# Kernel optimization log

Hardware: AMD Instinct MI355X
Metric: run time of the kernel (lower is better)

The kernel has to match this reference:

```python
import jax, jax.numpy as jnp
import numpy as np
import math

B, T, C, H = 4, 1024, 1024, 16
D = C // H
EPS = 1e-5

def layer_norm(x, gamma, beta):
    mu = jnp.mean(x, axis=-1, keepdims=True)
    var = jnp.var(x, axis=-1, keepdims=True)
    return (x - mu) * jax.lax.rsqrt(var + EPS) * gamma + beta

def setup_inputs() -> dict:
    key = jax.random.key(0)
    ks = jax.random.split(key, 12)
    s = 0.02
    return {
        "x": jax.random.normal(ks[0], (B, T, C), dtype=jnp.float32),
        "attn_mask": jax.random.randint(ks[1], (B, 1, 1, T), 0, 2, dtype=jnp.int32),
        "Wq": jax.random.normal(ks[2], (C, C), dtype=jnp.float32) * s,
        "bq": jnp.zeros((C,), dtype=jnp.float32),
        "Wk": jax.random.normal(ks[3], (C, C), dtype=jnp.float32) * s,
        "bk": jnp.zeros((C,), dtype=jnp.float32),
        "Wv": jax.random.normal(ks[4], (C, C), dtype=jnp.float32) * s,
        "bv": jnp.zeros((C,), dtype=jnp.float32),
        "Wo": jax.random.normal(ks[5], (C, C), dtype=jnp.float32) * s,
        "bo": jnp.zeros((C,), dtype=jnp.float32),
        "ln_g": jnp.ones((C,), dtype=jnp.float32),
        "ln_b": jnp.zeros((C,), dtype=jnp.float32),
    }

def reference(x, attn_mask, Wq, bq, Wk, bk, Wv, bv, Wo, bo, ln_g, ln_b):
    # projections -> [B, H, T, D]
    def split_heads(y):
        return y.reshape(B, T, H, D).transpose(0, 2, 1, 3)
    q = split_heads(x @ Wq + bq)
    k = split_heads(x @ Wk + bk)
    v = split_heads(x @ Wv + bv)
    scale = 1.0 / math.sqrt(D)
    wei = jnp.einsum('bhqd,bhkd->bhqk', q, k) * scale  # [B,H,T,T]
    wei = jnp.where(attn_mask == 0, jnp.float32(-jnp.inf), wei)
    wei = jax.nn.softmax(wei, axis=-1)
    out = jnp.einsum('bhqk,bhkd->bhqd', wei, v)
    out = out.transpose(0, 2, 1, 3).reshape(B, T, C)
    out = out @ Wo + bo
    return layer_norm(out, ln_g, ln_b)
```

## Files before the change

kernel.cpp:

```cpp
#include <hip/hip_runtime.h>
#include <hip/hip_bf16.h>
#include <stdint.h>

#define B_ 4
#define T_ 1024
#define C_ 1024
#define H_ 16
#define D_ 64
#define M_ 4096

typedef __attribute__((ext_vector_type(8))) short bf16x8;
typedef __attribute__((ext_vector_type(4))) float f32x4;
typedef __attribute__((ext_vector_type(4))) short short4v;

static __device__ __forceinline__ short f2bf(float f) {
  union { float f; unsigned u; } c; c.f = f;
  unsigned r = (c.u + 0x7fffu + ((c.u >> 16) & 1u)) >> 16;
  return (short)(unsigned short)r;
}

static __device__ __forceinline__ void gl2lds16(const void* g, void* l) {
  __builtin_amdgcn_global_load_lds(
      (const __attribute__((address_space(1))) void*)(uintptr_t)g,
      (__attribute__((address_space(3))) void*)(uint32_t)(uintptr_t)l,
      16, 0, 0);
}

__global__ __launch_bounds__(256) void k_prep(
    const float* __restrict__ x, short* __restrict__ xb,
    const float* __restrict__ Wq, const float* __restrict__ Wk,
    const float* __restrict__ Wv, const float* __restrict__ Wo,
    short* __restrict__ Wt) {
  __shared__ float t[32][33];
  const int id = blockIdx.x, tid = threadIdx.x;
  if (id < 4096) {
    int i = id * 256 + tid;
    float4 v = ((const float4*)x)[i];
    short4v o;
    o.x = f2bf(v.x); o.y = f2bf(v.y); o.z = f2bf(v.z); o.w = f2bf(v.w);
    ((short4v*)xb)[i] = o;
    return;
  }
  int j = id - 4096;
  int bz = j >> 10, r = j & 1023;
  int by = r >> 5, bx = r & 31;
  const float* W = (bz == 0) ? Wq : (bz == 1) ? Wk : (bz == 2) ? Wv : Wo;
  short* out = Wt + (size_t)bz * C_ * C_;
  int n0 = bx * 32, k0 = by * 32;
  int tx = tid & 31, ty = tid >> 5;
#pragma unroll
  for (int i = 0; i < 4; i++)
    t[ty + 8*i][tx] = W[(size_t)(k0 + ty + 8*i) * C_ + n0 + tx];
  __syncthreads();
#pragma unroll
  for (int i = 0; i < 4; i++)
    out[(size_t)(n0 + ty + 8*i) * C_ + k0 + tx] = f2bf(t[tx][ty + 8*i]);
}

static __device__ __forceinline__ void gemm_body(const short* __restrict__ A,
                                                 const short* __restrict__ Bt,
                                                 short* sA, short* sB,
                                                 f32x4 acc[4][4], int m0, int n0) {
  const int tid = threadIdx.x;
  const int w = tid >> 6, lane = tid & 63;
  const int quad = lane >> 4, l16 = lane & 15;
  const int wm = (w >> 1) * 64, wn = (w & 1) * 64;
  const int srow = lane >> 3;
  const int sch = lane & 7;

#pragma unroll
  for (int mt = 0; mt < 4; mt++)
#pragma unroll
    for (int nt = 0; nt < 4; nt++)
#pragma unroll
      for (int e = 0; e < 4; e++) acc[mt][nt][e] = 0.f;

  for (int k0 = 0; k0 < C_; k0 += 64) {
    __syncthreads();
#pragma unroll
    for (int i = 0; i < 4; i++) {
      int c = w * 4 + i;
      int row = c * 8 + srow;
      int ch = sch ^ (row & 7);
      gl2lds16(&A[(size_t)(m0 + row) * C_ + k0 + ch * 8], &sA[c * 512]);
      gl2lds16(&Bt[(size_t)(n0 + row) * C_ + k0 + ch * 8], &sB[c * 512]);
    }
    __syncthreads();
#pragma unroll
    for (int ks = 0; ks < 2; ks++) {
      bf16x8 af[4], bfv[4];
      int chq = ks * 4 + quad;
#pragma unroll
      for (int t4 = 0; t4 < 4; t4++) {
        int rowa = wm + t4 * 16 + l16;
        af[t4] = *(const bf16x8*)&sA[rowa * 64 + (chq ^ (rowa & 7)) * 8];
        int rowb = wn + t4 * 16 + l16;
        bfv[t4] = *(const bf16x8*)&sB[rowb * 64 + (chq ^ (rowb & 7)) * 8];
      }
#pragma unroll
      for (int mt = 0; mt < 4; mt++)
#pragma unroll
        for (int nt = 0; nt < 4; nt++)
          acc[mt][nt] = __builtin_amdgcn_mfma_f32_16x16x32_bf16(
              af[mt], bfv[nt], acc[mt][nt], 0, 0, 0);
    }
  }
}

__global__ __launch_bounds__(256, 3) void k_qkv(
    const short* __restrict__ A, const short* __restrict__ WtAll,
    const float* __restrict__ bq, const float* __restrict__ bk,
    const float* __restrict__ bv,
    short* __restrict__ Qb, short* __restrict__ Kb, short* __restrict__ Vtb) {
  __shared__ short sU[17408];
  const int id = blockIdx.x;
  const int mode = id % 3;
  const int j = id / 3;
  const int bx = j & 7, by = j >> 3;
  const int m0 = by * 128, n0 = bx * 128;
  const short* Bt = WtAll + (size_t)mode * C_ * C_;
  const float* bias = (mode == 0) ? bq : (mode == 1) ? bk : bv;
  f32x4 acc[4][4];
  gemm_body(A, Bt, sU, sU + 8192, acc, m0, n0);

  const int tid = threadIdx.x;
  const int w = tid >> 6, lane = tid & 63;
  const int quad = lane >> 4, l16 = lane & 15;
  const int wm = (w >> 1) * 64, wn = (w & 1) * 64;

  __syncthreads();
  if (mode < 2) {
#pragma unroll
    for (int nt = 0; nt < 4; nt++) {
      int nl = wn + nt * 16 + l16;
      float bval = bias[n0 + nl];
#pragma unroll
      for (int mt = 0; mt < 4; mt++)
#pragma unroll
        for (int r = 0; r < 4; r++)
          sU[(wm + mt * 16 + quad * 4 + r) * 136 + nl] = f2bf(acc[mt][nt][r] + bval);
    }
    __syncthreads();
    int dr = tid >> 1, hf = tid & 1;
    int mg = m0 + dr;
    int bb = mg >> 10, t = mg & 1023;
    int h = (n0 >> 6) + hf;
    short* dst = (mode == 0) ? Qb : Kb;
    size_t base = ((((size_t)(bb * H_ + h)) << 10) + t) * D_;
#pragma unroll
    for (int i = 0; i < 8; i++)
      *(int4*)&dst[base + i * 8] = *(const int4*)&sU[dr * 136 + hf * 64 + i * 8];
  } else {
#pragma unroll
    for (int nt = 0; nt < 4; nt++) {
      int nl = wn + nt * 16 + l16;
      float bval = bias[n0 + nl];
#pragma unroll
      for (int mt = 0; mt < 4; mt++)
#pragma unroll
        for (int r = 0; r < 4; r++)
          sU[nl * 136 + wm + mt * 16 + quad * 4 + r] = f2bf(acc[mt][nt][r] + bval);
    }
    __syncthreads();
    int dr = tid >> 1;
    int dg = n0 + dr, hd = dg >> 6, dl = dg & 63;
    int bb2 = m0 >> 10, t0 = m0 & 1023;
    size_t base = (((size_t)(bb2 * H_ + hd) * D_ + dl) << 10) + t0;
#pragma unroll
    for (int i = 0; i < 8; i++) {
      int jj = (tid & 1) * 8 + i;
      *(int4*)&Vtb[base + jj * 8] = *(const int4*)&sU[dr * 136 + jj * 8];
    }
  }
}

__global__ __launch_bounds__(256, 3) void k_proj(
    const short* __restrict__ A, const short* __restrict__ Bt,
    const float* __restrict__ bias, float* __restrict__ Y) {
  __shared__ short sA[4096];
  __shared__ short sB[8192];
  const int tid = threadIdx.x;
  const int w = tid >> 6, lane = tid & 63;
  const int quad = lane >> 4, l16 = lane & 15;
  const int m0 = blockIdx.y * 64, n0 = blockIdx.x * 128;
  const int wm = (w >> 1) * 32, wn = (w & 1) * 64;
  const int srow = lane >> 3, sch = lane & 7;

  f32x4 acc[2][4];
#pragma unroll
  for (int mt = 0; mt < 2; mt++)
#pragma unroll
    for (int nt = 0; nt < 4; nt++)
#pragma unroll
      for (int e = 0; e < 4; e++) acc[mt][nt][e] = 0.f;

  for (int k0 = 0; k0 < C_; k0 += 64) {
    __syncthreads();
#pragma unroll
    for (int i = 0; i < 6; i++) {
      int c = w * 6 + i;
      if (c < 8) {
        int row = c * 8 + srow;
        int ch = sch ^ (row & 7);
        gl2lds16(&A[(size_t)(m0 + row) * C_ + k0 + ch * 8], &sA[c * 512]);
      } else {
        int c2 = c - 8;
        int row = c2 * 8 + srow;
        int ch = sch ^ (row & 7);
        gl2lds16(&Bt[(size_t)(n0 + row) * C_ + k0 + ch * 8], &sB[c2 * 512]);
      }
    }
    __syncthreads();
#pragma unroll
    for (int ks = 0; ks < 2; ks++) {
      bf16x8 af[2], bfv[4];
      int chq = ks * 4 + quad;
#pragma unroll
      for (int t2 = 0; t2 < 2; t2++) {
        int rowa = wm + t2 * 16 + l16;
        af[t2] = *(const bf16x8*)&sA[rowa * 64 + (chq ^ (rowa & 7)) * 8];
      }
#pragma unroll
      for (int t4 = 0; t4 < 4; t4++) {
        int rowb = wn + t4 * 16 + l16;
        bfv[t4] = *(const bf16x8*)&sB[rowb * 64 + (chq ^ (rowb & 7)) * 8];
      }
#pragma unroll
      for (int mt = 0; mt < 2; mt++)
#pragma unroll
        for (int nt = 0; nt < 4; nt++)
          acc[mt][nt] = __builtin_amdgcn_mfma_f32_16x16x32_bf16(
              af[mt], bfv[nt], acc[mt][nt], 0, 0, 0);
    }
  }

#pragma unroll
  for (int mt = 0; mt < 2; mt++)
#pragma unroll
    for (int nt = 0; nt < 4; nt++) {
      int ng = n0 + wn + nt * 16 + l16;
      float bval = bias[ng];
#pragma unroll
      for (int r = 0; r < 4; r++) {
        int mg = m0 + wm + mt * 16 + quad * 4 + r;
        Y[(size_t)mg * C_ + ng] = acc[mt][nt][r] + bval;
      }
    }
}

#define PSTRIDE 136
__global__ __launch_bounds__(256, 2) void k_attn(
    const short* __restrict__ Qb, const short* __restrict__ Kb,
    const short* __restrict__ Vtb, const int* __restrict__ mask,
    short* __restrict__ Ob) {
  __shared__ short sK[8192];
  __shared__ short sV[8192];
  __shared__ short sP[4 * 32 * PSTRIDE];
  __shared__ float sBias[1024];
  const int tid = threadIdx.x;
  const int w = tid >> 6, lane = tid & 63;
  const int quad = lane >> 4, l16 = lane & 15;

  const int bx = blockIdx.x;
  const int xcd = bx & 7, j = bx >> 3;
  const int qb = j & 7, u = j >> 3;
  const int h = xcd * 2 + (u & 1), bb = u >> 1;
  const int tq0 = qb * 128 + w * 32;

  const short* Qh = Qb + ((size_t)(bb * H_ + h) << 10) * D_;
  const short* Kh = Kb + ((size_t)(bb * H_ + h) << 10) * D_;
  const short* Vh = Vtb + (((size_t)(bb * H_ + h) * D_) << 10);
  const int* mrow = mask + bb * T_;
  short* Pw = &sP[w * 32 * PSTRIDE];

  const float SC = 0.125f * 1.44269504088896340736f;

  {
    int4 m4 = ((const int4*)mrow)[tid];
    float4 bv4;
    bv4.x = m4.x ? 0.f : -1e30f; bv4.y = m4.y ? 0.f : -1e30f;
    bv4.z = m4.z ? 0.f : -1e30f; bv4.w = m4.w ? 0.f : -1e30f;
    ((float4*)sBias)[tid] = bv4;
  }

  bf16x8 aq[2][2];
#pragma unroll
  for (int rt = 0; rt < 2; rt++)
#pragma unroll
    for (int ks = 0; ks < 2; ks++)
      aq[rt][ks] = *(const bf16x8*)&Qh[(size_t)(tq0 + rt * 16 + l16) * D_ +
                                       ks * 32 + quad * 8];

  bf16x8 ones8;
#pragma unroll
  for (int e = 0; e < 8; e++) ones8[e] = (short)0x3F80;

  f32x4 o[2][4];
  f32x4 osum[2];
#pragma unroll
  for (int rt = 0; rt < 2; rt++) {
#pragma unroll
    for (int nt = 0; nt < 4; nt++)
#pragma unroll
      for (int e = 0; e < 4; e++) o[rt][nt][e] = 0.f;
#pragma unroll
    for (int e = 0; e < 4; e++) osum[rt][e] = 0.f;
  }

  for (int kt = 0; kt < T_; kt += 128) {
    __syncthreads();
#pragma unroll
    for (int i2 = 0; i2 < 4; i2++) {
      int i = w * 4 + i2;
      int row = i * 8 + (lane >> 3);
      int g = (lane & 7) ^ (row & 7);
      gl2lds16(&Kh[(size_t)(kt + row) * D_ + g * 8], &sK[i * 512]);
    }
#pragma unroll
    for (int i2 = 0; i2 < 4; i2++) {
      int i = w * 4 + i2;
      int row = i * 4 + (lane >> 4);
      int g = (lane & 15) ^ (row & 15);
      gl2lds16(&Vh[((size_t)row << 10) + kt + g * 8], &sV[i * 512]);
    }
    __syncthreads();

    f32x4 s[2][8];
#pragma unroll
    for (int rt = 0; rt < 2; rt++)
#pragma unroll
      for (int ct = 0; ct < 8; ct++)
#pragma unroll
        for (int e = 0; e < 4; e++) s[rt][ct][e] = 0.f;

#pragma unroll
    for (int ks = 0; ks < 2; ks++)
#pragma unroll
      for (int ct = 0; ct < 8; ct++) {
        int rowb = ct * 16 + l16;
        bf16x8 bk8 = *(const bf16x8*)&sK[rowb * 64 +
                                         (((ks * 4 + quad) ^ (rowb & 7)) * 8)];
        s[0][ct] = __builtin_amdgcn_mfma_f32_16x16x32_bf16(aq[0][ks], bk8, s[0][ct], 0, 0, 0);
        s[1][ct] = __builtin_amdgcn_mfma_f32_16x16x32_bf16(aq[1][ks], bk8, s[1][ct], 0, 0, 0);
      }

    float mb[8];
#pragma unroll
    for (int ct = 0; ct < 8; ct++) mb[ct] = sBias[kt + ct * 16 + l16];

#pragma unroll
    for (int rt = 0; rt < 2; rt++)
#pragma unroll
      for (int ct = 0; ct < 8; ct++) {
        float p0 = __builtin_amdgcn_exp2f(fmaf(s[rt][ct][0], SC, mb[ct]));
        float p1 = __builtin_amdgcn_exp2f(fmaf(s[rt][ct][1], SC, mb[ct]));
        float p2 = __builtin_amdgcn_exp2f(fmaf(s[rt][ct][2], SC, mb[ct]));
        float p3 = __builtin_amdgcn_exp2f(fmaf(s[rt][ct][3], SC, mb[ct]));
        __hip_bfloat162 h01 = __float22bfloat162_rn(make_float2(p0, p1));
        __hip_bfloat162 h23 = __float22bfloat162_rn(make_float2(p2, p3));
        unsigned u01 = *(unsigned*)&h01;
        unsigned u23 = *(unsigned*)&h23;
        int base = (rt * 16 + quad * 4) * PSTRIDE + ct * 16 + l16;
        Pw[base] = (short)(u01 & 0xffffu);
        Pw[base + PSTRIDE] = (short)(u01 >> 16);
        Pw[base + 2 * PSTRIDE] = (short)(u23 & 0xffffu);
        Pw[base + 3 * PSTRIDE] = (short)(u23 >> 16);
      }

#pragma unroll
    for (int ks2 = 0; ks2 < 4; ks2++) {
      bf16x8 pa0 = *(const bf16x8*)&Pw[l16 * PSTRIDE + ks2 * 32 + quad * 8];
      bf16x8 pa1 = *(const bf16x8*)&Pw[(16 + l16) * PSTRIDE + ks2 * 32 + quad * 8];
      osum[0] = __builtin_amdgcn_mfma_f32_16x16x32_bf16(pa0, ones8, osum[0], 0, 0, 0);
      osum[1] = __builtin_amdgcn_mfma_f32_16x16x32_bf16(pa1, ones8, osum[1], 0, 0, 0);
#pragma unroll
      for (int nt = 0; nt < 4; nt++) {
        int rowv = nt * 16 + l16;
        bf16x8 bv8 = *(const bf16x8*)&sV[rowv * 128 +
                                         (((ks2 * 4 + quad) ^ (rowv & 15)) * 8)];
        o[0][nt] = __builtin_amdgcn_mfma_f32_16x16x32_bf16(pa0, bv8, o[0][nt], 0, 0, 0);
        o[1][nt] = __builtin_amdgcn_mfma_f32_16x16x32_bf16(pa1, bv8, o[1][nt], 0, 0, 0);
      }
    }
  }

#pragma unroll
  for (int rt = 0; rt < 2; rt++)
#pragma unroll
    for (int r = 0; r < 4; r++) {
      float inv = 1.f / osum[rt][r];
      int tg = tq0 + rt * 16 + quad * 4 + r;
#pragma unroll
      for (int nt = 0; nt < 4; nt++) {
        int col = h * D_ + nt * 16 + l16;
        Ob[(size_t)(bb * T_ + tg) * C_ + col] = f2bf(o[rt][nt][r] * inv);
      }
    }
}

__global__ __launch_bounds__(256) void k_ln(float* __restrict__ Y,
                                            const float* __restrict__ g,
                                            const float* __restrict__ b) {
  const int w = threadIdx.x >> 6, lane = threadIdx.x & 63;
  const int row = blockIdx.x * 4 + w;
  float4* yp = (float4*)(Y + (size_t)row * C_);
  float4 v[4];
#pragma unroll
  for (int i = 0; i < 4; i++) v[i] = yp[i * 64 + lane];

  float sm = 0.f;
#pragma unroll
  for (int i = 0; i < 4; i++) sm += v[i].x + v[i].y + v[i].z + v[i].w;
#pragma unroll
  for (int off = 32; off; off >>= 1) sm += __shfl_xor(sm, off);
  float mu = sm * (1.f / C_);

  float q = 0.f;
#pragma unroll
  for (int i = 0; i < 4; i++) {
    float dx = v[i].x - mu, dy = v[i].y - mu, dz = v[i].z - mu, dw = v[i].w - mu;
    q += dx * dx + dy * dy + dz * dz + dw * dw;
  }
#pragma unroll
  for (int off = 32; off; off >>= 1) q += __shfl_xor(q, off);
  float rsq = rsqrtf(q * (1.f / C_) + 1e-5f);

#pragma unroll
  for (int i = 0; i < 4; i++) {
    float4 gg = ((const float4*)g)[i * 64 + lane];
    float4 bb = ((const float4*)b)[i * 64 + lane];
    float4 out;
    out.x = (v[i].x - mu) * rsq * gg.x + bb.x;
    out.y = (v[i].y - mu) * rsq * gg.y + bb.y;
    out.z = (v[i].z - mu) * rsq * gg.z + bb.z;
    out.w = (v[i].w - mu) * rsq * gg.w + bb.w;
    yp[i * 64 + lane] = out;
  }
}

extern "C" void kernel_launch(void* const* d_in, const int* in_sizes, int n_in,
                              void* d_out, int out_size, void* d_ws, size_t ws_size,
                              hipStream_t stream) {
  (void)in_sizes; (void)n_in; (void)out_size; (void)ws_size;
  const float* x    = (const float*)d_in[0];
  const int*   mask = (const int*)d_in[1];
  const float* Wq   = (const float*)d_in[2];
  const float* bq   = (const float*)d_in[3];
  const float* Wk   = (const float*)d_in[4];
  const float* bk   = (const float*)d_in[5];
  const float* Wv   = (const float*)d_in[6];
  const float* bv   = (const float*)d_in[7];
  const float* Wo   = (const float*)d_in[8];
  const float* bo   = (const float*)d_in[9];
  const float* lng  = (const float*)d_in[10];
  const float* lnb  = (const float*)d_in[11];

  char* ws = (char*)d_ws;
  short* xb  = (short*)(ws);
  short* Wt  = (short*)(ws + ((size_t)8  << 20));
  short* Qb  = (short*)(ws + ((size_t)16 << 20));
  short* Kb  = (short*)(ws + ((size_t)24 << 20));
  short* Vtb = (short*)(ws + ((size_t)32 << 20));
  short* Ob  = xb;
  float* Y   = (float*)d_out;

  k_prep<<<dim3(8192), dim3(256), 0, stream>>>(x, xb, Wq, Wk, Wv, Wo, Wt);
  k_qkv<<<dim3(768), dim3(256), 0, stream>>>(xb, Wt, bq, bk, bv, Qb, Kb, Vtb);
  k_attn<<<dim3(512), dim3(256), 0, stream>>>(Qb, Kb, Vtb, mask, Ob);
  k_proj<<<dim3(8, 64), dim3(256), 0, stream>>>(Ob, Wt + (size_t)3 * C_ * C_, bo, Y);
  k_ln<<<dim3(1024), dim3(256), 0, stream>>>(Y, lng, lnb);
}
```

Measured before the change: 183.3 us.

## Compact unmasked keys and values to skip masked attention tiles

Computes a prefix-sum compaction of the key mask in the prep kernel, then gathers only unmasked K and V rows into compacted buffers. The attention loop then runs only over the padded count of valid keys, roughly halving the work for a random mask. This adds an extra gather kernel and an indirect-indexed V gather that reads scattered elements.

```diff
diff --git a/kernel.cpp b/kernel.cpp
--- a/kernel.cpp
+++ b/kernel.cpp
@@ -30,8 +30,10 @@
     const float* __restrict__ x, short* __restrict__ xb,
     const float* __restrict__ Wq, const float* __restrict__ Wk,
     const float* __restrict__ Wv, const float* __restrict__ Wo,
-    short* __restrict__ Wt) {
+    short* __restrict__ Wt, const int* __restrict__ mask,
+    int* __restrict__ tmap, float* __restrict__ bc, int* __restrict__ np) {
   __shared__ float t[32][33];
+  __shared__ int wsum[4];
   const int id = blockIdx.x, tid = threadIdx.x;
   if (id < 4096) {
     int i = id * 256 + tid;
@@ -41,20 +43,94 @@
     ((short4v*)xb)[i] = o;
     return;
   }
-  int j = id - 4096;
-  int bz = j >> 10, r = j & 1023;
-  int by = r >> 5, bx = r & 31;
-  const float* W = (bz == 0) ? Wq : (bz == 1) ? Wk : (bz == 2) ? Wv : Wo;
-  short* out = Wt + (size_t)bz * C_ * C_;
-  int n0 = bx * 32, k0 = by * 32;
-  int tx = tid & 31, ty = tid >> 5;
-#pragma unroll
-  for (int i = 0; i < 4; i++)
-    t[ty + 8*i][tx] = W[(size_t)(k0 + ty + 8*i) * C_ + n0 + tx];
+  if (id < 8192) {
+    int j = id - 4096;
+    int bz = j >> 10, r = j & 1023;
+    int by = r >> 5, bx = r & 31;
+    const float* W = (bz == 0) ? Wq : (bz == 1) ? Wk : (bz == 2) ? Wv : Wo;
+    short* out = Wt + (size_t)bz * C_ * C_;
+    int n0 = bx * 32, k0 = by * 32;
+    int tx = tid & 31, ty = tid >> 5;
+#pragma unroll
+    for (int i = 0; i < 4; i++)
+      t[ty + 8*i][tx] = W[(size_t)(k0 + ty + 8*i) * C_ + n0 + tx];
+    __syncthreads();
+#pragma unroll
+    for (int i = 0; i < 4; i++)
+      out[(size_t)(n0 + ty + 8*i) * C_ + k0 + tx] = f2bf(t[tx][ty + 8*i]);
+    return;
+  }
+  const int b = id - 8192;
+  const int lane = tid & 63, w = tid >> 6;
+  int4 m = ((const int4*)(mask + b * T_))[tid];
+  int cnt = (m.x ? 1 : 0) + (m.y ? 1 : 0) + (m.z ? 1 : 0) + (m.w ? 1 : 0);
+  int v = cnt;
+#pragma unroll
+  for (int off = 1; off < 64; off <<= 1) {
+    int u = __shfl_up(v, off);
+    if (lane >= off) v += u;
+  }
+  if (lane == 63) wsum[w] = v;
+  int4 z4; z4.x = 0; z4.y = 0; z4.z = 0; z4.w = 0;
+  ((int4*)(tmap + b * T_))[tid] = z4;
+  float4 neg; neg.x = -1e30f; neg.y = -1e30f; neg.z = -1e30f; neg.w = -1e30f;
+  ((float4*)(bc + b * T_))[tid] = neg;
   __syncthreads();
-#pragma unroll
-  for (int i = 0; i < 4; i++)
-    out[(size_t)(n0 + ty + 8*i) * C_ + k0 + tx] = f2bf(t[tx][ty + 8*i]);
+  int base = 0;
+#pragma unroll
+  for (int i = 0; i < 4; i++) if (i < w) base += wsum[i];
+  int incl = base + v;
+  int c = incl - cnt;
+  int t0 = tid * 4;
+  if (m.x) { tmap[b * T_ + c] = t0;     bc[b * T_ + c] = 0.f; c++; }
+  if (m.y) { tmap[b * T_ + c] = t0 + 1; bc[b * T_ + c] = 0.f; c++; }
+  if (m.z) { tmap[b * T_ + c] = t0 + 2; bc[b * T_ + c] = 0.f; c++; }
+  if (m.w) { tmap[b * T_ + c] = t0 + 3; bc[b * T_ + c] = 0.f; c++; }
+  if (tid == 255) np[b] = (incl + 127) & ~127;
+}
+
+__global__ __launch_bounds__(256) void k_gather(
+    const short* __restrict__ Kb, const short* __restrict__ Vtb,
+    const int* __restrict__ tmap, const int* __restrict__ np,
+    short* __restrict__ Kc, short* __restrict__ Vc) {
+  const int blk = blockIdx.x, tid = threadIdx.x;
+  const int bh = blk >> 3, chunk = blk & 7;
+  const int b = bh >> 4, h = bh & 15;
+  const int c0 = chunk * 128;
+  if (c0 >= np[b]) return;
+  const int* tmr = tmap + b * T_;
+
+  {
+    int dr = tid >> 1, hf = tid & 1;
+    int c = c0 + dr;
+    int t = tmr[c];
+    const short* src = Kb + ((((size_t)(b * H_ + h)) << 10) + t) * D_ + hf * 32;
+    short* dst = Kc + ((((size_t)(b * H_ + h)) << 10) + c) * D_ + hf * 32;
+#pragma unroll
+    for (int i = 0; i < 4; i++)
+      ((int4*)dst)[i] = ((const int4*)src)[i];
+  }
+
+  {
+    int d = tid >> 2, sub = tid & 3;
+    int cbase = c0 + sub * 32;
+    const short* src = Vtb + (((size_t)(b * H_ + h) * D_ + d) << 10);
+    short* dst = Vc + (((size_t)(b * H_ + h) * D_ + d) << 10) + cbase;
+    int tm[32];
+#pragma unroll
+    for (int q = 0; q < 8; q++) {
+      int4 t4 = ((const int4*)(tmr + cbase))[q];
+      tm[q * 4 + 0] = t4.x; tm[q * 4 + 1] = t4.y;
+      tm[q * 4 + 2] = t4.z; tm[q * 4 + 3] = t4.w;
+    }
+#pragma unroll
+    for (int q = 0; q < 8; q++) {
+      short4v s4;
+      s4.x = src[tm[q * 4 + 0]]; s4.y = src[tm[q * 4 + 1]];
+      s4.z = src[tm[q * 4 + 2]]; s4.w = src[tm[q * 4 + 3]];
+      ((short4v*)dst)[q] = s4;
+    }
+  }
 }
 
 static __device__ __forceinline__ void gemm_body(const short* __restrict__ A,
@@ -250,9 +326,9 @@
 
 #define PSTRIDE 136
 __global__ __launch_bounds__(256, 2) void k_attn(
-    const short* __restrict__ Qb, const short* __restrict__ Kb,
-    const short* __restrict__ Vtb, const int* __restrict__ mask,
-    short* __restrict__ Ob) {
+    const short* __restrict__ Qb, const short* __restrict__ Kc,
+    const short* __restrict__ Vc, const float* __restrict__ bc,
+    const int* __restrict__ np, short* __restrict__ Ob) {
   __shared__ short sK[8192];
   __shared__ short sV[8192];
   __shared__ short sP[4 * 32 * PSTRIDE];
@@ -268,20 +344,14 @@
   const int tq0 = qb * 128 + w * 32;
 
   const short* Qh = Qb + ((size_t)(bb * H_ + h) << 10) * D_;
-  const short* Kh = Kb + ((size_t)(bb * H_ + h) << 10) * D_;
-  const short* Vh = Vtb + (((size_t)(bb * H_ + h) * D_) << 10);
-  const int* mrow = mask + bb * T_;
+  const short* Kh = Kc + ((size_t)(bb * H_ + h) << 10) * D_;
+  const short* Vh = Vc + (((size_t)(bb * H_ + h) * D_) << 10);
   short* Pw = &sP[w * 32 * PSTRIDE];
+  const int npb = np[bb];
 
   const float SC = 0.125f * 1.44269504088896340736f;
 
-  {
-    int4 m4 = ((const int4*)mrow)[tid];
-    float4 bv4;
-    bv4.x = m4.x ? 0.f : -1e30f; bv4.y = m4.y ? 0.f : -1e30f;
-    bv4.z = m4.z ? 0.f : -1e30f; bv4.w = m4.w ? 0.f : -1e30f;
-    ((float4*)sBias)[tid] = bv4;
-  }
+  ((float4*)sBias)[tid] = ((const float4*)(bc + bb * T_))[tid];
 
   bf16x8 aq[2][2];
 #pragma unroll
@@ -307,7 +377,7 @@
     for (int e = 0; e < 4; e++) osum[rt][e] = 0.f;
   }
 
-  for (int kt = 0; kt < T_; kt += 128) {
+  for (int kt = 0; kt < npb; kt += 128) {
     __syncthreads();
 #pragma unroll
     for (int i2 = 0; i2 < 4; i2++) {
@@ -456,17 +526,24 @@
   const float* lnb  = (const float*)d_in[11];
 
   char* ws = (char*)d_ws;
-  short* xb  = (short*)(ws);
-  short* Wt  = (short*)(ws + ((size_t)8  << 20));
-  short* Qb  = (short*)(ws + ((size_t)16 << 20));
-  short* Kb  = (short*)(ws + ((size_t)24 << 20));
-  short* Vtb = (short*)(ws + ((size_t)32 << 20));
-  short* Ob  = xb;
-  float* Y   = (float*)d_out;
-
-  k_prep<<<dim3(8192), dim3(256), 0, stream>>>(x, xb, Wq, Wk, Wv, Wo, Wt);
+  short* xb   = (short*)(ws);
+  short* Wt   = (short*)(ws + ((size_t)8  << 20));
+  short* Qb   = (short*)(ws + ((size_t)16 << 20));
+  short* Kb   = (short*)(ws + ((size_t)24 << 20));
+  short* Vtb  = (short*)(ws + ((size_t)32 << 20));
+  short* Kc   = (short*)(ws + ((size_t)40 << 20));
+  short* Vc   = (short*)(ws + ((size_t)48 << 20));
+  int*   tmap = (int*)(ws + ((size_t)56 << 20));
+  float* bc   = (float*)(ws + ((size_t)57 << 20));
+  int*   np   = (int*)(ws + ((size_t)58 << 20));
+  short* Ob   = xb;
+  float* Y    = (float*)d_out;
+
+  k_prep<<<dim3(8196), dim3(256), 0, stream>>>(x, xb, Wq, Wk, Wv, Wo, Wt,
+                                               mask, tmap, bc, np);
   k_qkv<<<dim3(768), dim3(256), 0, stream>>>(xb, Wt, bq, bk, bv, Qb, Kb, Vtb);
-  k_attn<<<dim3(512), dim3(256), 0, stream>>>(Qb, Kb, Vtb, mask, Ob);
+  k_gather<<<dim3(512), dim3(256), 0, stream>>>(Kb, Vtb, tmap, np, Kc, Vc);
+  k_attn<<<dim3(512), dim3(256), 0, stream>>>(Qb, Kc, Vc, bc, np, Ob);
   k_proj<<<dim3(8, 64), dim3(256), 0, stream>>>(Ob, Wt + (size_t)3 * C_ * C_, bo, Y);
   k_ln<<<dim3(1024), dim3(256), 0, stream>>>(Y, lng, lnb);
 }
```

Result: slower. 193.1 us (+5.4%).
